# Optimization experiments

Hardware: AMD Instinct MI355X
Metric: run time of the kernel (lower is better)

## Reference

```python
import jax, jax.numpy as jnp
import numpy as np

B, S, D, H, HD = 2, 2048, 1024, 16, 64
K, L = 1024, 4  # num_codes, vq_levels


def setup_inputs() -> dict:
    key = jax.random.key(0)
    ks = jax.random.split(key, 12)
    w = lambda k, shape: jax.random.normal(k, shape, jnp.float32) * 0.02
    return {
        "x": jax.random.normal(ks[0], (B, S, D), jnp.float32),
        "ln1_g": jnp.ones((D,), jnp.float32), "ln1_b": jnp.zeros((D,), jnp.float32),
        "wq": w(ks[1], (D, D)), "wk": w(ks[2], (D, D)), "wv": w(ks[3], (D, D)),
        "wg": w(ks[4], (D, D)), "wo": w(ks[5], (D, D)),
        "ln2_g": jnp.ones((D,), jnp.float32), "ln2_b": jnp.zeros((D,), jnp.float32),
        "w1": w(ks[6], (D, 4 * D)), "b1": jnp.zeros((4 * D,), jnp.float32),
        "w2": w(ks[7], (4 * D, D)), "b2": jnp.zeros((D,), jnp.float32),
        "ln3_g": jnp.ones((D,), jnp.float32), "ln3_b": jnp.zeros((D,), jnp.float32),
        "codebooks": jax.random.uniform(ks[8], (L, K, D), jnp.float32, -1.0 / K, 1.0 / K),
    }


def _ln(x, g, b):
    m = jnp.mean(x, -1, keepdims=True)
    v = jnp.var(x, -1, keepdims=True)
    return (x - m) / jnp.sqrt(v + 1e-5) * g + b


def _rope(x):  # x: [B, S, H, HD]
    hd = x.shape[-1]
    inv = 1.0 / (10000.0 ** (jnp.arange(0, hd, 2, dtype=jnp.float32) / hd))
    t = jnp.arange(x.shape[1], dtype=jnp.float32)
    f = jnp.einsum('i,j->ij', t, inv)               # [S, HD/2]
    emb = jnp.concatenate([f, f], -1)               # [S, HD]
    cos = jnp.cos(emb)[None, :, None, :]
    sin = jnp.sin(emb)[None, :, None, :]
    x1, x2 = jnp.split(x, 2, -1)
    rot = jnp.concatenate([-x2, x1], -1)
    return x * cos + rot * sin


def reference(x, ln1_g, ln1_b, wq, wk, wv, wg, wo, ln2_g, ln2_b,
              w1, b1, w2, b2, ln3_g, ln3_b, codebooks):
    # --- retention sub-block (pre-LN) ---
    h = _ln(x, ln1_g, ln1_b)
    q = (h @ wq).reshape(B, S, H, HD)
    k = (h @ wk).reshape(B, S, H, HD)
    v = (h @ wv).reshape(B, S, H, HD)
    q, k = _rope(q), _rope(k)
    q, k, v = (a.transpose(0, 2, 1, 3) for a in (q, k, v))  # [B,H,S,HD]
    i = jnp.arange(S)
    dmask = jnp.tril(i[:, None] - i[None, :]).astype(jnp.float32)  # [S,S], >=0
    gamma = (1.0 - jnp.exp2(-5.0 - jnp.arange(H, dtype=jnp.float32)))[:, None, None]
    decay = (gamma ** dmask) * jnp.tril(jnp.ones((S, S), jnp.float32))  # [H,S,S]
    ret = jnp.einsum('bhqd,bhkd->bhqk', q, k) / np.sqrt(HD).astype(np.float32) * decay
    o = jnp.einsum('bhqk,bhkd->bhqd', ret, v).transpose(0, 2, 1, 3).reshape(B, S, D)
    g = jax.nn.silu(h @ wg)
    x = x + (o * g) @ wo
    # --- MLP sub-block (pre-LN) ---
    h2 = _ln(x, ln2_g, ln2_b)
    x = x + (jax.nn.gelu(h2 @ w1 + b1, approximate=False) @ w2 + b2)
    # --- residual vector quantizer ---
    xn = _ln(x, ln3_g, ln3_b)
    residual, total = xn, jnp.zeros_like(xn)
    ql, el = 0.0, 0.0
    for lvl in range(L):
        cb = codebooks[lvl]                         # [K, D]
        flat = residual.reshape(-1, D)              # [B*S, D]
        d2 = (jnp.sum(flat ** 2, 1, keepdims=True)
              + jnp.sum(cb ** 2, 1) - 2.0 * flat @ cb.T)
        idx = jnp.argmin(d2, 1)
        quant = cb[idx].reshape(xn.shape)
        ql = ql + jnp.mean((quant - jax.lax.stop_gradient(residual)) ** 2)
        el = el + jnp.mean((jax.lax.stop_gradient(quant) - residual) ** 2)
        total = total + quant
        residual = residual - jax.lax.stop_gradient(quant)
    final = xn + jax.lax.stop_gradient(total - xn)  # straight-through
    return (x + final, ql / L, el / L)
```

## Files before the change

kernel.cpp:

```cpp
#include <hip/hip_runtime.h>
#include <cstdint>
#include <cstddef>

#define DEV __device__ __forceinline__

typedef __attribute__((ext_vector_type(8))) short bf16x8;
typedef __attribute__((ext_vector_type(4))) float f32x4;

typedef const __attribute__((address_space(1))) void gl_void;
typedef __attribute__((address_space(3))) void lds_void;

DEV unsigned short f2bf(float f){
  union { float f; uint32_t u; } v; v.f = f;
  uint32_t r = v.u + 0x7FFFu + ((v.u >> 16) & 1u);
  return (unsigned short)(r >> 16);
}
DEV float bf2f(unsigned short u){
  union { uint32_t u; float f; } v; v.u = ((uint32_t)u) << 16; return v.f;
}
DEV uint32_t packbf2(float a, float b){
  return (uint32_t)f2bf(a) | ((uint32_t)f2bf(b) << 16);
}

__global__ void ln_kernel(const float* __restrict__ x, const float* __restrict__ gw,
                          const float* __restrict__ bw, unsigned short* __restrict__ obf,
                          float* __restrict__ of32)
{
  const int row = blockIdx.x, t = threadIdx.x;
  const float4 v = ((const float4*)(x + (size_t)row*1024))[t];
  float s  = v.x + v.y + v.z + v.w;
  float s2 = v.x*v.x + v.y*v.y + v.z*v.z + v.w*v.w;
  #pragma unroll
  for (int o = 32; o >= 1; o >>= 1){ s += __shfl_down(s, o); s2 += __shfl_down(s2, o); }
  __shared__ float red[8];
  const int w = t >> 6, ln = t & 63;
  if (ln == 0){ red[w] = s; red[4+w] = s2; }
  __syncthreads();
  const float fs  = red[0]+red[1]+red[2]+red[3];
  const float fs2 = red[4]+red[5]+red[6]+red[7];
  const float mean = fs * (1.0f/1024.0f);
  const float var  = fs2 * (1.0f/1024.0f) - mean*mean;
  const float rstd = rsqrtf(var + 1e-5f);
  const float4 gv = ((const float4*)gw)[t];
  const float4 bv = ((const float4*)bw)[t];
  float4 o4;
  o4.x = (v.x-mean)*rstd*gv.x + bv.x;
  o4.y = (v.y-mean)*rstd*gv.y + bv.y;
  o4.z = (v.z-mean)*rstd*gv.z + bv.z;
  o4.w = (v.w-mean)*rstd*gv.w + bv.w;
  if (of32) ((float4*)(of32 + (size_t)row*1024))[t] = o4;
  ushort4 ob; ob.x = f2bf(o4.x); ob.y = f2bf(o4.y); ob.z = f2bf(o4.z); ob.w = f2bf(o4.w);
  ((ushort4*)(obf + (size_t)row*1024))[t] = ob;
}

struct Ptr5 { const float* p[5]; };
__global__ void transpose_cvt5(Ptr5 in, unsigned short* __restrict__ out)
{
  __shared__ float tile[32][33];
  const float* src = in.p[blockIdx.z];
  unsigned short* dst = out + (size_t)blockIdx.z*1048576;
  const int c0 = blockIdx.x*32, r0 = blockIdx.y*32;
  const int tx = threadIdx.x & 31, ty = threadIdx.x >> 5;
  #pragma unroll
  for (int i = 0; i < 32; i += 8)
    tile[ty+i][tx] = src[(size_t)(r0+ty+i)*1024 + c0 + tx];
  __syncthreads();
  #pragma unroll
  for (int i = 0; i < 32; i += 8)
    dst[(size_t)(c0+ty+i)*1024 + r0 + tx] = f2bf(tile[tx][ty+i]);
}

__global__ void transpose_cvt(const float* __restrict__ in, unsigned short* __restrict__ out,
                              int R, int C)
{
  __shared__ float tile[32][33];
  const int c0 = blockIdx.x*32, r0 = blockIdx.y*32;
  const int tx = threadIdx.x & 31, ty = threadIdx.x >> 5;
  #pragma unroll
  for (int i = 0; i < 32; i += 8)
    tile[ty+i][tx] = in[(size_t)(r0+ty+i)*C + c0 + tx];
  __syncthreads();
  #pragma unroll
  for (int i = 0; i < 32; i += 8)
    out[(size_t)(c0+ty+i)*R + r0 + tx] = f2bf(tile[tx][ty+i]);
}

__global__ void cvtnorm_kernel(const float* __restrict__ cb, unsigned short* __restrict__ cbbf,
                               float* __restrict__ cbn2)
{
  const int code = blockIdx.x, t = threadIdx.x;
  const float4 v = ((const float4*)(cb + (size_t)code*1024))[t];
  ushort4 o; o.x = f2bf(v.x); o.y = f2bf(v.y); o.z = f2bf(v.z); o.w = f2bf(v.w);
  ((ushort4*)(cbbf + (size_t)code*1024))[t] = o;
  float s = v.x*v.x + v.y*v.y + v.z*v.z + v.w*v.w;
  #pragma unroll
  for (int off = 32; off >= 1; off >>= 1) s += __shfl_down(s, off);
  __shared__ float red[4];
  if ((t & 63) == 0) red[t >> 6] = s;
  __syncthreads();
  if (t == 0) cbn2[code] = red[0]+red[1]+red[2]+red[3];
}

__global__ void rope_tab(float2* __restrict__ rt)
{
  const int i = blockIdx.x*256 + threadIdx.x;
  const int s = i >> 5, j = i & 31;
  const float ang = (float)s * exp2f(-(float)j * 0.4152410118609203f);
  float sn, cs; sincosf(ang, &sn, &cs);
  rt[i] = make_float2(cs, sn);
}

template<int EPI>
__global__ __launch_bounds__(512, 2) void gemm256(
    const unsigned short* __restrict__ A, const unsigned short* __restrict__ BT,
    unsigned short* __restrict__ C, const float* __restrict__ bias,
    const float2* __restrict__ rt, int M, int N, int K)
{
  __shared__ __align__(16) unsigned short SH[65536];
  const int t = threadIdx.x;
  const int w = t >> 6, ln = t & 63, lg = ln >> 4, lc = ln & 15;
  const int wm = w >> 2, wn = w & 3;
  const int gx = gridDim.x, nwg = gridDim.x * gridDim.y;
  int lin = blockIdx.y * gx + blockIdx.x;
  lin = (lin >> 3) + (lin & 7) * (nwg >> 3);
  const int m0 = (lin / gx) * 256, n0 = (lin % gx) * 256;
  const int nkt = K >> 6;

  f32x4 acc[8][4] = {};

  auto stage = [&](int buf, int kt, int half, int isB){
    const unsigned short* src = isB ? BT : A;
    const int mb = isB ? n0 : m0;
    #pragma unroll
    for (int j = 0; j < 2; ++j){
      const int u = j*512 + t;
      const int ro = u >> 3;
      const int k16 = (u & 7) ^ (ro & 7);
      __builtin_amdgcn_global_load_lds(
        (gl_void*)(src + (size_t)(mb + half*128 + ro)*K + (size_t)kt*64 + k16*8),
        (lds_void*)&SH[buf*32768 + isB*16384 + half*8192 + (j*512 + (t & ~63))*8],
        16, 0, 0);
    }
  };

  auto ldA = [&](int buf, int mf, int ks) -> bf16x8 {
    const int R = wm*128 + mf*16 + lc;
    const int ci = (ks*32 + lg*8) ^ ((lc & 7) << 3);
    return *(const bf16x8*)&SH[buf*32768 + R*64 + ci];
  };
  auto ldB = [&](int buf, int nf, int ks) -> bf16x8 {
    const int R = wn*64 + nf*16 + lc;
    const int ci = (ks*32 + lg*8) ^ ((lc & 7) << 3);
    return *(const bf16x8*)&SH[buf*32768 + 16384 + R*64 + ci];
  };

  stage(0, 0, 0, 0); stage(0, 0, 1, 0); stage(0, 0, 0, 1); stage(0, 0, 1, 1);
  asm volatile("s_waitcnt vmcnt(0)" ::: "memory");
  __builtin_amdgcn_s_barrier();

  bf16x8 aF[4][2], bF[2][2];
  for (int kt = 0; kt < nkt; ++kt){
    const int cur = kt & 1;
    const bool pf = (kt + 1 < nkt);

    #pragma unroll
    for (int f = 0; f < 4; ++f){ aF[f][0] = ldA(cur, f, 0); aF[f][1] = ldA(cur, f, 1); }
    #pragma unroll
    for (int f = 0; f < 2; ++f){ bF[f][0] = ldB(cur, f, 0); bF[f][1] = ldB(cur, f, 1); }
    if (pf){ stage(cur^1, kt+1, 0, 0); stage(cur^1, kt+1, 0, 1); }
    __builtin_amdgcn_s_barrier();
    __builtin_amdgcn_s_setprio(1);
    #pragma unroll
    for (int mf = 0; mf < 4; ++mf)
      #pragma unroll
      for (int nf = 0; nf < 2; ++nf){
        acc[mf][nf] = __builtin_amdgcn_mfma_f32_16x16x32_bf16(aF[mf][0], bF[nf][0], acc[mf][nf], 0, 0, 0);
        acc[mf][nf] = __builtin_amdgcn_mfma_f32_16x16x32_bf16(aF[mf][1], bF[nf][1], acc[mf][nf], 0, 0, 0);
      }
    __builtin_amdgcn_s_setprio(0);
    __builtin_amdgcn_s_barrier();

    #pragma unroll
    for (int f = 0; f < 2; ++f){ bF[f][0] = ldB(cur, 2+f, 0); bF[f][1] = ldB(cur, 2+f, 1); }
    if (pf){ stage(cur^1, kt+1, 1, 1); stage(cur^1, kt+1, 1, 0); }
    __builtin_amdgcn_s_barrier();
    __builtin_amdgcn_s_setprio(1);
    #pragma unroll
    for (int mf = 0; mf < 4; ++mf)
      #pragma unroll
      for (int nf = 0; nf < 2; ++nf){
        acc[mf][2+nf] = __builtin_amdgcn_mfma_f32_16x16x32_bf16(aF[mf][0], bF[nf][0], acc[mf][2+nf], 0, 0, 0);
        acc[mf][2+nf] = __builtin_amdgcn_mfma_f32_16x16x32_bf16(aF[mf][1], bF[nf][1], acc[mf][2+nf], 0, 0, 0);
      }
    __builtin_amdgcn_s_setprio(0);
    __builtin_amdgcn_s_barrier();

    #pragma unroll
    for (int f = 0; f < 4; ++f){ aF[f][0] = ldA(cur, 4+f, 0); aF[f][1] = ldA(cur, 4+f, 1); }
    __builtin_amdgcn_s_barrier();
    __builtin_amdgcn_s_setprio(1);
    #pragma unroll
    for (int mf = 0; mf < 4; ++mf)
      #pragma unroll
      for (int nf = 0; nf < 2; ++nf){
        acc[4+mf][2+nf] = __builtin_amdgcn_mfma_f32_16x16x32_bf16(aF[mf][0], bF[nf][0], acc[4+mf][2+nf], 0, 0, 0);
        acc[4+mf][2+nf] = __builtin_amdgcn_mfma_f32_16x16x32_bf16(aF[mf][1], bF[nf][1], acc[4+mf][2+nf], 0, 0, 0);
      }
    __builtin_amdgcn_s_setprio(0);
    __builtin_amdgcn_s_barrier();

    #pragma unroll
    for (int f = 0; f < 2; ++f){ bF[f][0] = ldB(cur, f, 0); bF[f][1] = ldB(cur, f, 1); }
    __builtin_amdgcn_s_barrier();
    __builtin_amdgcn_s_setprio(1);
    #pragma unroll
    for (int mf = 0; mf < 4; ++mf)
      #pragma unroll
      for (int nf = 0; nf < 2; ++nf){
        acc[4+mf][nf] = __builtin_amdgcn_mfma_f32_16x16x32_bf16(aF[mf][0], bF[nf][0], acc[4+mf][nf], 0, 0, 0);
        acc[4+mf][nf] = __builtin_amdgcn_mfma_f32_16x16x32_bf16(aF[mf][1], bF[nf][1], acc[4+mf][nf], 0, 0, 0);
      }
    __builtin_amdgcn_s_setprio(0);
    asm volatile("s_waitcnt vmcnt(0)" ::: "memory");
    __builtin_amdgcn_s_barrier();
  }

  const int mrow = m0 + wm*128, ncol = n0 + wn*64;
  if constexpr (EPI == 3){
    const int sect = ncol >> 10;
    unsigned short* outp = C + (size_t)sect*4194304;
    #pragma unroll
    for (int mf = 0; mf < 8; ++mf){
      #pragma unroll
      for (int r = 0; r < 4; ++r){
        const int row = mrow + mf*16 + lg*4 + r;
        const int s_ = row & 2047;
        #pragma unroll
        for (int nf = 0; nf < 4; ++nf){
          const int c1 = (ncol + nf*16 + lc) & 1023;
          float v = acc[mf][nf][r];
          if (sect <= 1){
            const float2 cs = rt[(s_ << 5) + (c1 & 31)];
            const float vp = acc[mf][nf ^ 2][r];
            v = (c1 & 32) ? (v*cs.x + vp*cs.y) : (v*cs.x - vp*cs.y);
          } else if (sect == 3){
            v = v * (1.0f / (1.0f + __expf(-v)));
          }
          outp[(size_t)row*1024 + c1] = f2bf(v);
        }
      }
    }
  } else {
    #pragma unroll
    for (int mf = 0; mf < 8; ++mf){
      #pragma unroll
      for (int r = 0; r < 4; ++r){
        const int row = mrow + mf*16 + lg*4 + r;
        #pragma unroll
        for (int nf = 0; nf < 4; ++nf){
          const int col = ncol + nf*16 + lc;
          float v = acc[mf][nf][r] + bias[col];
          v = 0.5f * v * (1.0f + erff(v * 0.70710678118654752f));
          C[(size_t)row*N + col] = f2bf(v);
        }
      }
    }
  }
}

template<int EPI, bool BIAS, bool RES, bool OUTBF, int NSPLIT>
__global__ __launch_bounds__(256, 3) void gemm64_bt(
    const unsigned short* __restrict__ A, const unsigned short* __restrict__ BT,
    void* __restrict__ Cv, const float* __restrict__ bias, const float* __restrict__ resid,
    int M, int N, int K)
{
  __shared__ __align__(16) unsigned short As[2][64*64];
  __shared__ __align__(16) unsigned short Bs[2][128*64];
  const int t = threadIdx.x;
  const int w = t >> 6, ln = t & 63, lg = ln >> 4, lc = ln & 15;
  const int gx = gridDim.x, nwg = gridDim.x * gridDim.y;
  int lin = blockIdx.y * gx + blockIdx.x;
  lin = (lin >> 3) + (lin & 7) * (nwg >> 3);
  const int bx = lin % gx, by = lin / gx;
  const int m0 = by * 64, n0 = bx * 128;
  const int wr = (w >> 1) * 32, wc = (w & 1) * 64;
  f32x4 acc[2][4] = {};
  const int nkt = (K >> 6) / NSPLIT;
  const int ktb = (NSPLIT > 1) ? blockIdx.z * nkt : 0;

  auto stage = [&](int buf, int kt){
    #pragma unroll
    for (int c = 0; c < 2; ++c){
      const int chunk = c*256 + t;
      const int row = chunk >> 3;
      const int kb = (((chunk & 7) << 4) ^ ((row & 7) << 4)) >> 1;
      __builtin_amdgcn_global_load_lds(
          (gl_void*)(A + (size_t)(m0+row)*K + (size_t)(ktb+kt)*64 + kb),
          (lds_void*)&As[buf][(c*256 + w*64)*8], 16, 0, 0);
    }
    #pragma unroll
    for (int c = 0; c < 4; ++c){
      const int chunk = c*256 + t;
      const int row = chunk >> 3;
      const int kb = (((chunk & 7) << 4) ^ ((row & 7) << 4)) >> 1;
      __builtin_amdgcn_global_load_lds(
          (gl_void*)(BT + (size_t)(n0+row)*K + (size_t)(ktb+kt)*64 + kb),
          (lds_void*)&Bs[buf][(c*256 + w*64)*8], 16, 0, 0);
    }
  };

  stage(0, 0);
  __syncthreads();
  for (int kt = 0; kt < nkt; ++kt){
    const int cur = kt & 1;
    if (kt + 1 < nkt) stage(cur ^ 1, kt + 1);
    #pragma unroll
    for (int ks = 0; ks < 2; ++ks){
      bf16x8 af[2], bfr[4];
      #pragma unroll
      for (int i = 0; i < 2; ++i){
        const int rowA = wr + i*16 + lc;
        const int colA = (((ks<<6) + (lg<<4)) ^ ((rowA & 7) << 4)) >> 1;
        af[i] = *(const bf16x8*)&As[cur][rowA*64 + colA];
      }
      #pragma unroll
      for (int i = 0; i < 4; ++i){
        const int rowB = wc + i*16 + lc;
        const int colB = (((ks<<6) + (lg<<4)) ^ ((rowB & 7) << 4)) >> 1;
        bfr[i] = *(const bf16x8*)&Bs[cur][rowB*64 + colB];
      }
      #pragma unroll
      for (int m = 0; m < 2; ++m)
        #pragma unroll
        for (int n = 0; n < 4; ++n)
          acc[m][n] = __builtin_amdgcn_mfma_f32_16x16x32_bf16(af[m], bfr[n], acc[m][n], 0, 0, 0);
    }
    __syncthreads();
  }

  if constexpr (EPI == 4){
    #pragma unroll
    for (int m = 0; m < 2; ++m){
      #pragma unroll
      for (int r = 0; r < 4; ++r){
        float best = 3.4e38f; int bi = 0;
        #pragma unroll
        for (int n = 0; n < 4; ++n){
          const int col = n0 + wc + n*16 + lc;
          const float d = bias[col] - 2.0f*acc[m][n][r];
          if (d < best){ best = d; bi = col; }
        }
        #pragma unroll
        for (int o = 1; o < 16; o <<= 1){
          const float ob = __shfl_xor(best, o);
          const int oi = __shfl_xor(bi, o);
          if (ob < best || (ob == best && oi < bi)){ best = ob; bi = oi; }
        }
        if (lc == 0){
          const int row = m0 + wr + m*16 + lg*4 + r;
          ((float2*)Cv)[row*16 + bx*2 + (w & 1)] = make_float2(best, (float)bi);
        }
      }
    }
    return;
  }

  float* Cp = (float*)Cv + (NSPLIT > 1 ? (size_t)blockIdx.z * (size_t)M * N : 0);
  #pragma unroll
  for (int m = 0; m < 2; ++m){
    #pragma unroll
    for (int n = 0; n < 4; ++n){
      #pragma unroll
      for (int r = 0; r < 4; ++r){
        const int row = m0 + wr + m*16 + lg*4 + r;
        const int col = n0 + wc + n*16 + lc;
        float v = acc[m][n][r];
        if constexpr (BIAS) v += bias[col];
        if constexpr (RES) v += resid[(size_t)row*N + col];
        if constexpr (OUTBF) ((unsigned short*)Cv)[(size_t)row*N + col] = f2bf(v);
        else                 Cp[(size_t)row*N + col] = v;
      }
    }
  }
}

__global__ void splitk_reduce(const float* __restrict__ p, const float* __restrict__ bias,
                              const float* __restrict__ resid, float* __restrict__ out)
{
  const int i = blockIdx.x*256 + threadIdx.x;
  const float4 a = ((const float4*)p)[i];
  const float4 b = ((const float4*)(p + 4194304))[i];
  const float4 rv = ((const float4*)resid)[i];
  const float4 bv = ((const float4*)bias)[i & 255];
  float4 o;
  o.x = a.x + b.x + rv.x + bv.x;
  o.y = a.y + b.y + rv.y + bv.y;
  o.z = a.z + b.z + rv.z + bv.z;
  o.w = a.w + b.w + rv.w + bv.w;
  ((float4*)out)[i] = o;
}

__global__ __launch_bounds__(256, 2) void chunk_sum(
    const unsigned short* __restrict__ kb, const unsigned short* __restrict__ vb,
    float* __restrict__ Tbuf)
{
  __shared__ unsigned short KT[64*72];
  __shared__ unsigned short VT[64*72];
  const int t = threadIdx.x, w = t >> 6, ln = t & 63, lg = ln >> 4, lc = ln & 15;
  const int blk = blockIdx.x;
  const int bh = blk >> 5, c = blk & 31;
  const int b = bh >> 4, hh = bh & 15;
  const float lg2g = log2f(1.0f - exp2f(-5.0f - (float)hh));
  #pragma unroll
  for (int ch = 0; ch < 2; ++ch){
    const int chunk = ch*256 + t;
    const int i = chunk >> 3, d0 = (chunk & 7)*8;
    const size_t gofs = ((size_t)(b*2048 + c*64 + i))*1024 + hh*64 + d0;
    const float wi = exp2f(lg2g * (float)(64 - i));
    union {uint4 u; unsigned short s[8];} kv, vv;
    kv.u = *(const uint4*)(kb + gofs);
    vv.u = *(const uint4*)(vb + gofs);
    #pragma unroll
    for (int j = 0; j < 8; ++j){
      KT[(d0+j)*72 + i] = f2bf(bf2f(kv.s[j]) * wi);
      VT[(d0+j)*72 + i] = vv.s[j];
    }
  }
  __syncthreads();
  f32x4 acc[4] = {};
  #pragma unroll
  for (int ks = 0; ks < 2; ++ks){
    const bf16x8 af = *(const bf16x8*)&KT[(w*16 + lc)*72 + ks*32 + lg*8];
    #pragma unroll
    for (int n = 0; n < 4; ++n){
      const bf16x8 bf = *(const bf16x8*)&VT[(n*16 + lc)*72 + ks*32 + lg*8];
      acc[n] = __builtin_amdgcn_mfma_f32_16x16x32_bf16(af, bf, acc[n], 0, 0, 0);
    }
  }
  float* out = Tbuf + (size_t)blk*4096;
  #pragma unroll
  for (int n = 0; n < 4; ++n)
    #pragma unroll
    for (int r = 0; r < 4; ++r)
      out[(w*16 + lg*4 + r)*64 + n*16 + lc] = acc[n][r];
}

__global__ void chunk_scan(const float* __restrict__ Tbuf, unsigned short* __restrict__ statesT)
{
  const int bh = blockIdx.x, t = threadIdx.x;
  const int hh = bh & 15;
  const float gamma = 1.0f - exp2f(-5.0f - (float)hh);
  const float g64 = exp2f(log2f(gamma) * 64.0f);
  float S[16];
  #pragma unroll
  for (int j = 0; j < 16; ++j) S[j] = 0.f;
  const int dv = t >> 2, d0 = (t & 3) * 16;
  for (int c = 0; c < 32; ++c){
    const size_t base = ((size_t)(bh*32 + c))*4096;
    union { unsigned short s[8]; uint4 u; } p0, p1;
    #pragma unroll
    for (int j = 0; j < 8; ++j){ p0.s[j] = f2bf(S[j]); p1.s[j] = f2bf(S[8+j]); }
    *(uint4*)(statesT + base + t*16)     = p0.u;
    *(uint4*)(statesT + base + t*16 + 8) = p1.u;
    #pragma unroll
    for (int j = 0; j < 16; ++j)
      S[j] = g64*S[j] + Tbuf[base + (size_t)(d0 + j)*64 + dv];
  }
}

__global__ __launch_bounds__(256, 2) void retention_chunk(
    const unsigned short* __restrict__ qb, const unsigned short* __restrict__ kb,
    const unsigned short* __restrict__ vb, const unsigned short* __restrict__ gb,
    const unsigned short* __restrict__ statesT, unsigned short* __restrict__ og)
{
  __shared__ unsigned short VT[64*72];
  __shared__ unsigned short Pw[64*72];
  const int t = threadIdx.x, w = t >> 6, ln = t & 63, lg = ln >> 4, lc = ln & 15;
  const int blk = blockIdx.x;
  const int bh = blk >> 5, c = blk & 31;
  const int b = bh >> 4, hh = bh & 15;
  const float lg2g = log2f(1.0f - exp2f(-5.0f - (float)hh));
  float gpr[4];
  #pragma unroll
  for (int r = 0; r < 4; ++r) gpr[r] = exp2f(-lg2g * (float)r);
  const size_t rowbase = (size_t)(b*2048 + c*64);

  #pragma unroll
  for (int ch = 0; ch < 2; ++ch){
    const int chunk = ch*256 + t;
    const int i = chunk >> 3, d0 = (chunk & 7)*8;
    union {uint4 u; unsigned short s[8];} vv;
    vv.u = *(const uint4*)(vb + (rowbase + i)*1024 + hh*64 + d0);
    #pragma unroll
    for (int j = 0; j < 8; ++j) VT[(d0+j)*72 + i] = vv.s[j];
  }

  bf16x8 Qf[2], Kf[4][2];
  #pragma unroll
  for (int ks = 0; ks < 2; ++ks){
    union {uint4 u; bf16x8 f;} cv;
    cv.u = *(const uint4*)(qb + (rowbase + w*16 + lc)*1024 + hh*64 + ks*32 + lg*8);
    Qf[ks] = cv.f;
    #pragma unroll
    for (int mt = 0; mt < 4; ++mt){
      union {uint4 u; bf16x8 f;} kv;
      kv.u = *(const uint4*)(kb + (rowbase + mt*16 + lc)*1024 + hh*64 + ks*32 + lg*8);
      Kf[mt][ks] = kv.f;
    }
  }

  f32x4 st[4] = {};
  #pragma unroll
  for (int ks = 0; ks < 2; ++ks)
    #pragma unroll
    for (int mt = 0; mt < 4; ++mt)
      st[mt] = __builtin_amdgcn_mfma_f32_16x16x32_bf16(Kf[mt][ks], Qf[ks], st[mt], 0, 0, 0);

  __syncthreads();

  #pragma unroll
  for (int mt = 0; mt < 4; ++mt){
    const int kp = mt*16 + lg*4;
    const int qrow = w*16 + lc;
    const int delta0 = qrow - kp;
    const float dec0 = exp2f(lg2g * (float)delta0) * 0.125f;
    float vals[4];
    #pragma unroll
    for (int r = 0; r < 4; ++r)
      vals[r] = (delta0 >= r) ? st[mt][r] * dec0 * gpr[r] : 0.0f;
    uint2 pk; pk.x = packbf2(vals[0], vals[1]); pk.y = packbf2(vals[2], vals[3]);
    *(uint2*)&Pw[qrow*72 + kp] = pk;
  }

  f32x4 acc[4] = {};
  const unsigned short* Sbase = statesT + (size_t)blk*4096;
  #pragma unroll
  for (int ks = 0; ks < 2; ++ks)
    #pragma unroll
    for (int n = 0; n < 4; ++n){
      union {uint4 u; bf16x8 f;} sv;
      sv.u = *(const uint4*)(Sbase + (n*16 + lc)*64 + ks*32 + lg*8);
      acc[n] = __builtin_amdgcn_mfma_f32_16x16x32_bf16(Qf[ks], sv.f, acc[n], 0, 0, 0);
    }
  #pragma unroll
  for (int n = 0; n < 4; ++n)
    #pragma unroll
    for (int r = 0; r < 4; ++r)
      acc[n][r] *= exp2f(lg2g * (float)(w*16 + lg*4 + r)) * 0.125f;

  #pragma unroll
  for (int ks = 0; ks < 2; ++ks){
    const bf16x8 Pf = *(const bf16x8*)&Pw[(w*16 + lc)*72 + ks*32 + lg*8];
    #pragma unroll
    for (int n = 0; n < 4; ++n){
      const bf16x8 Vf = *(const bf16x8*)&VT[(n*16 + lc)*72 + ks*32 + lg*8];
      acc[n] = __builtin_amdgcn_mfma_f32_16x16x32_bf16(Pf, Vf, acc[n], 0, 0, 0);
    }
  }

  #pragma unroll
  for (int n = 0; n < 4; ++n){
    #pragma unroll
    for (int r = 0; r < 4; ++r){
      const size_t row = rowbase + w*16 + lg*4 + r;
      const int col = hh*64 + n*16 + lc;
      const float gv = bf2f(gb[row*1024 + col]);
      og[row*1024 + col] = f2bf(acc[n][r] * gv);
    }
  }
}

__global__ void rvq_update3(const float* __restrict__ cb_l, const float2* __restrict__ partials,
                            const float* __restrict__ res_in, float* __restrict__ res_out,
                            unsigned short* __restrict__ resb, float* __restrict__ qlpart, int lvl)
{
  const int m = blockIdx.x, t = threadIdx.x;
  __shared__ int sid;
  if (t == 0){
    float best = 3.4e38f; int bi = 0;
    #pragma unroll
    for (int p = 0; p < 16; ++p){
      const float2 pr = partials[m*16 + p];
      if (pr.x < best){ best = pr.x; bi = (int)pr.y; }
    }
    sid = bi;
  }
  __syncthreads();
  const int id = sid;
  const float4 qv = ((const float4*)(cb_l + (size_t)id*1024))[t];
  const float4 rv = ((const float4*)(res_in + (size_t)m*1024))[t];
  float4 nr; nr.x = rv.x - qv.x; nr.y = rv.y - qv.y; nr.z = rv.z - qv.z; nr.w = rv.w - qv.w;
  ((float4*)(res_out + (size_t)m*1024))[t] = nr;
  ushort4 nb; nb.x = f2bf(nr.x); nb.y = f2bf(nr.y); nb.z = f2bf(nr.z); nb.w = f2bf(nr.w);
  ((ushort4*)(resb + (size_t)m*1024))[t] = nb;
  float s = nr.x*nr.x + nr.y*nr.y + nr.z*nr.z + nr.w*nr.w;
  #pragma unroll
  for (int o = 32; o >= 1; o >>= 1) s += __shfl_down(s, o);
  __shared__ float red[4];
  if ((t & 63) == 0) red[t >> 6] = s;
  __syncthreads();
  if (t == 0) qlpart[lvl*4096 + m] = red[0]+red[1]+red[2]+red[3];
}

__global__ void final_add3(const float* __restrict__ x2, const float* __restrict__ xn,
                           const float* __restrict__ res4, float* __restrict__ out)
{
  const int i = blockIdx.x*256 + threadIdx.x;
  const float4 a = ((const float4*)x2)[i];
  const float4 b = ((const float4*)xn)[i];
  const float4 c = ((const float4*)res4)[i];
  float4 o;
  o.x = a.x + b.x - c.x;
  o.y = a.y + b.y - c.y;
  o.z = a.z + b.z - c.z;
  o.w = a.w + b.w - c.w;
  ((float4*)out)[i] = o;
}

__global__ void ql_final(const float* __restrict__ qlpart, float* __restrict__ outs)
{
  const int t = threadIdx.x;
  float s = 0.f;
  for (int i = t; i < 16384; i += 256) s += qlpart[i];
  #pragma unroll
  for (int o = 32; o >= 1; o >>= 1) s += __shfl_down(s, o);
  __shared__ float red[4];
  if ((t & 63) == 0) red[t >> 6] = s;
  __syncthreads();
  if (t == 0){
    const float q = (red[0]+red[1]+red[2]+red[3]) * (1.0f/4194304.0f) * 0.25f;
    outs[0] = q; outs[1] = q;
  }
}

extern "C" void kernel_launch(void* const* d_in, const int* in_sizes, int n_in,
                              void* d_out, int out_size, void* d_ws, size_t ws_size,
                              hipStream_t stream)
{
  const float* x     = (const float*)d_in[0];
  const float* ln1_g = (const float*)d_in[1];
  const float* ln1_b = (const float*)d_in[2];
  const float* wq    = (const float*)d_in[3];
  const float* wk    = (const float*)d_in[4];
  const float* wv    = (const float*)d_in[5];
  const float* wg    = (const float*)d_in[6];
  const float* wo    = (const float*)d_in[7];
  const float* ln2_g = (const float*)d_in[8];
  const float* ln2_b = (const float*)d_in[9];
  const float* w1    = (const float*)d_in[10];
  const float* b1    = (const float*)d_in[11];
  const float* w2    = (const float*)d_in[12];
  const float* b2    = (const float*)d_in[13];
  const float* ln3_g = (const float*)d_in[14];
  const float* ln3_b = (const float*)d_in[15];
  const float* cb    = (const float*)d_in[16];

  char* ws = (char*)d_ws;
  const size_t MB = 1024*1024;
  unsigned short* wqkvgT = (unsigned short*)(ws + 0*MB);
  unsigned short* w1T  = (unsigned short*)(ws + 10*MB);
  unsigned short* w2T  = (unsigned short*)(ws + 18*MB);
  unsigned short* cbbf = (unsigned short*)(ws + 26*MB);
  float* cbn2     = (float*)(ws + 34*MB);
  float* qlpart   = (float*)(ws + 34*MB + 16*1024);
  float2* partials= (float2*)(ws + 34*MB + 128*1024);
  unsigned short* hbf  = (unsigned short*)(ws + 35*MB);
  unsigned short* qbuf = (unsigned short*)(ws + 43*MB);
  unsigned short* kbuf = (unsigned short*)(ws + 51*MB);
  unsigned short* vbuf = (unsigned short*)(ws + 59*MB);
  unsigned short* gbuf = (unsigned short*)(ws + 67*MB);
  float* skbuf  = (float*)(ws + 43*MB);
  unsigned short* ogb  = (unsigned short*)(ws + 75*MB);
  float* x1     = (float*)(ws + 83*MB);
  unsigned short* h2   = (unsigned short*)(ws + 99*MB);
  unsigned short* a1   = (unsigned short*)(ws + 107*MB);
  float* x2     = (float*)(ws + 139*MB);
  float* Tbuf   = (float*)(ws + 139*MB);
  float* xnf    = (float*)(ws + 155*MB);
  unsigned short* statesT = (unsigned short*)(ws + 155*MB);
  unsigned short* resb = (unsigned short*)(ws + 171*MB);
  float2* rtab  = (float2*)(ws + 179*MB);
  float* resw   = (float*)(ws + 187*MB);

  float* outf = (float*)d_out;

  Ptr5 p5; p5.p[0]=wq; p5.p[1]=wk; p5.p[2]=wv; p5.p[3]=wg; p5.p[4]=wo;
  hipLaunchKernelGGL(transpose_cvt5, dim3(32,32,5), dim3(256), 0, stream, p5, wqkvgT);
  hipLaunchKernelGGL(transpose_cvt, dim3(128,32), dim3(256), 0, stream, w1, w1T, 1024, 4096);
  hipLaunchKernelGGL(transpose_cvt, dim3(32,128), dim3(256), 0, stream, w2, w2T, 4096, 1024);
  hipLaunchKernelGGL(cvtnorm_kernel, dim3(4096), dim3(256), 0, stream, cb, cbbf, cbn2);
  hipLaunchKernelGGL(rope_tab, dim3(256), dim3(256), 0, stream, rtab);

  hipLaunchKernelGGL(ln_kernel, dim3(4096), dim3(256), 0, stream, x, ln1_g, ln1_b, hbf, (float*)nullptr);
  hipLaunchKernelGGL((gemm256<3>), dim3(16,16), dim3(512), 0, stream,
                     hbf, wqkvgT, qbuf, (const float*)nullptr, (const float2*)rtab, 4096, 4096, 1024);
  hipLaunchKernelGGL(chunk_sum,  dim3(1024), dim3(256), 0, stream, kbuf, vbuf, Tbuf);
  hipLaunchKernelGGL(chunk_scan, dim3(32),   dim3(256), 0, stream, Tbuf, statesT);
  hipLaunchKernelGGL(retention_chunk, dim3(1024), dim3(256), 0, stream,
                     qbuf, kbuf, vbuf, gbuf, statesT, ogb);
  hipLaunchKernelGGL((gemm64_bt<0,false,true,false,1>), dim3(8,64), dim3(256), 0, stream,
                     ogb, wqkvgT + 4194304, (void*)x1, (const float*)nullptr, x, 4096, 1024, 1024);

  hipLaunchKernelGGL(ln_kernel, dim3(4096), dim3(256), 0, stream, x1, ln2_g, ln2_b, h2, (float*)nullptr);
  hipLaunchKernelGGL((gemm256<2>), dim3(16,16), dim3(512), 0, stream,
                     h2, w1T, a1, b1, (const float2*)rtab, 4096, 4096, 1024);
  hipLaunchKernelGGL((gemm64_bt<0,false,false,false,2>), dim3(8,64,2), dim3(256), 0, stream,
                     a1, w2T, (void*)skbuf, (const float*)nullptr, (const float*)nullptr, 4096, 1024, 4096);
  hipLaunchKernelGGL(splitk_reduce, dim3(4096), dim3(256), 0, stream, skbuf, b2, x1, x2);

  hipLaunchKernelGGL(ln_kernel, dim3(4096), dim3(256), 0, stream, x2, ln3_g, ln3_b, resb, xnf);
  for (int lvl = 0; lvl < 4; ++lvl){
    hipLaunchKernelGGL((gemm64_bt<4,false,false,false,1>), dim3(8,64), dim3(256), 0, stream,
                       resb, cbbf + (size_t)lvl*1048576, (void*)partials,
                       cbn2 + lvl*1024, (const float*)nullptr, 4096, 1024, 1024);
    hipLaunchKernelGGL(rvq_update3, dim3(4096), dim3(256), 0, stream,
                       cb + (size_t)lvl*1048576, partials,
                       (lvl == 0) ? xnf : resw, resw, resb, qlpart, lvl);
  }

  hipLaunchKernelGGL(final_add3, dim3(4096), dim3(256), 0, stream, x2, xnf, resw, outf);
  hipLaunchKernelGGL(ql_final, dim3(1), dim3(256), 0, stream, qlpart, outf + 4194304);
}
```

Baseline: 435.9 us.

## Triple-buffer GEMM LDS stages with two-ahead prefetch and partial vmcnt waits

New measurement: 446.4 us. 1.02x slower.

```diff
diff --git a/kernel.cpp b/kernel.cpp
--- a/kernel.cpp
+++ b/kernel.cpp
@@ -116,7 +116,7 @@
     unsigned short* __restrict__ C, const float* __restrict__ bias,
     const float2* __restrict__ rt, int M, int N, int K)
 {
-  __shared__ __align__(16) unsigned short SH[65536];
+  __shared__ __align__(16) unsigned short SH[49152];
   const int t = threadIdx.x;
   const int w = t >> 6, ln = t & 63, lg = ln >> 4, lc = ln & 15;
   const int wm = w >> 2, wn = w & 3;
@@ -124,104 +124,75 @@
   int lin = blockIdx.y * gx + blockIdx.x;
   lin = (lin >> 3) + (lin & 7) * (nwg >> 3);
   const int m0 = (lin / gx) * 256, n0 = (lin % gx) * 256;
-  const int nkt = K >> 6;
+  const int nkt = K >> 5;
 
   f32x4 acc[8][4] = {};
 
-  auto stage = [&](int buf, int kt, int half, int isB){
-    const unsigned short* src = isB ? BT : A;
-    const int mb = isB ? n0 : m0;
-    #pragma unroll
-    for (int j = 0; j < 2; ++j){
-      const int u = j*512 + t;
-      const int ro = u >> 3;
-      const int k16 = (u & 7) ^ (ro & 7);
-      __builtin_amdgcn_global_load_lds(
-        (gl_void*)(src + (size_t)(mb + half*128 + ro)*K + (size_t)kt*64 + k16*8),
-        (lds_void*)&SH[buf*32768 + isB*16384 + half*8192 + (j*512 + (t & ~63))*8],
-        16, 0, 0);
+  auto stage = [&](int buf, int kt){
+    #pragma unroll
+    for (int isB = 0; isB < 2; ++isB){
+      const unsigned short* src = isB ? BT : A;
+      const int mb = isB ? n0 : m0;
+      #pragma unroll
+      for (int j = 0; j < 2; ++j){
+        const int u = j*512 + t;
+        const int ro = u >> 2;
+        const int su = (u & 3) ^ ((ro >> 1) & 3);
+        __builtin_amdgcn_global_load_lds(
+          (gl_void*)(src + (size_t)(mb + ro)*K + (size_t)kt*32 + su*8),
+          (lds_void*)&SH[buf*16384 + isB*8192 + (j*512 + (t & ~63))*8],
+          16, 0, 0);
+      }
     }
   };
 
-  auto ldA = [&](int buf, int mf, int ks) -> bf16x8 {
+  auto ldA = [&](int buf, int mf) -> bf16x8 {
     const int R = wm*128 + mf*16 + lc;
-    const int ci = (ks*32 + lg*8) ^ ((lc & 7) << 3);
-    return *(const bf16x8*)&SH[buf*32768 + R*64 + ci];
+    const int cu = lg ^ ((R >> 1) & 3);
+    return *(const bf16x8*)&SH[buf*16384 + (R*4 + cu)*8];
   };
-  auto ldB = [&](int buf, int nf, int ks) -> bf16x8 {
+  auto ldB = [&](int buf, int nf) -> bf16x8 {
     const int R = wn*64 + nf*16 + lc;
-    const int ci = (ks*32 + lg*8) ^ ((lc & 7) << 3);
-    return *(const bf16x8*)&SH[buf*32768 + 16384 + R*64 + ci];
+    const int cu = lg ^ ((R >> 1) & 3);
+    return *(const bf16x8*)&SH[buf*16384 + 8192 + (R*4 + cu)*8];
   };
 
-  stage(0, 0, 0, 0); stage(0, 0, 1, 0); stage(0, 0, 0, 1); stage(0, 0, 1, 1);
-  asm volatile("s_waitcnt vmcnt(0)" ::: "memory");
+  stage(0, 0); stage(1, 1);
+  asm volatile("s_waitcnt vmcnt(4)" ::: "memory");
   __builtin_amdgcn_s_barrier();
 
-  bf16x8 aF[4][2], bF[2][2];
   for (int kt = 0; kt < nkt; ++kt){
-    const int cur = kt & 1;
-    const bool pf = (kt + 1 < nkt);
-
-    #pragma unroll
-    for (int f = 0; f < 4; ++f){ aF[f][0] = ldA(cur, f, 0); aF[f][1] = ldA(cur, f, 1); }
-    #pragma unroll
-    for (int f = 0; f < 2; ++f){ bF[f][0] = ldB(cur, f, 0); bF[f][1] = ldB(cur, f, 1); }
-    if (pf){ stage(cur^1, kt+1, 0, 0); stage(cur^1, kt+1, 0, 1); }
+    const int cur = kt % 3;
+    const bool pf = (kt + 2 < nkt);
+    bf16x8 aF[4], bF[4];
+
+    if (pf) stage((kt + 2) % 3, kt + 2);
+    #pragma unroll
+    for (int f = 0; f < 4; ++f){ aF[f] = ldA(cur, f); bF[f] = ldB(cur, f); }
     __builtin_amdgcn_s_barrier();
     __builtin_amdgcn_s_setprio(1);
     #pragma unroll
     for (int mf = 0; mf < 4; ++mf)
       #pragma unroll
-      for (int nf = 0; nf < 2; ++nf){
-        acc[mf][nf] = __builtin_amdgcn_mfma_f32_16x16x32_bf16(aF[mf][0], bF[nf][0], acc[mf][nf], 0, 0, 0);
-        acc[mf][nf] = __builtin_amdgcn_mfma_f32_16x16x32_bf16(aF[mf][1], bF[nf][1], acc[mf][nf], 0, 0, 0);
-      }
+      for (int nf = 0; nf < 4; ++nf)
+        acc[mf][nf] = __builtin_amdgcn_mfma_f32_16x16x32_bf16(aF[mf], bF[nf], acc[mf][nf], 0, 0, 0);
     __builtin_amdgcn_s_setprio(0);
+    asm volatile("s_waitcnt lgkmcnt(0)" ::: "memory");
     __builtin_amdgcn_s_barrier();
 
     #pragma unroll
-    for (int f = 0; f < 2; ++f){ bF[f][0] = ldB(cur, 2+f, 0); bF[f][1] = ldB(cur, 2+f, 1); }
-    if (pf){ stage(cur^1, kt+1, 1, 1); stage(cur^1, kt+1, 1, 0); }
+    for (int f = 0; f < 4; ++f) aF[f] = ldA(cur, 4 + f);
     __builtin_amdgcn_s_barrier();
     __builtin_amdgcn_s_setprio(1);
     #pragma unroll
     for (int mf = 0; mf < 4; ++mf)
       #pragma unroll
-      for (int nf = 0; nf < 2; ++nf){
-        acc[mf][2+nf] = __builtin_amdgcn_mfma_f32_16x16x32_bf16(aF[mf][0], bF[nf][0], acc[mf][2+nf], 0, 0, 0);
-        acc[mf][2+nf] = __builtin_amdgcn_mfma_f32_16x16x32_bf16(aF[mf][1], bF[nf][1], acc[mf][2+nf], 0, 0, 0);
-      }
+      for (int nf = 0; nf < 4; ++nf)
+        acc[4+mf][nf] = __builtin_amdgcn_mfma_f32_16x16x32_bf16(aF[mf], bF[nf], acc[4+mf][nf], 0, 0, 0);
     __builtin_amdgcn_s_setprio(0);
-    __builtin_amdgcn_s_barrier();
-
-    #pragma unroll
-    for (int f = 0; f < 4; ++f){ aF[f][0] = ldA(cur, 4+f, 0); aF[f][1] = ldA(cur, 4+f, 1); }
-    __builtin_amdgcn_s_barrier();
-    __builtin_amdgcn_s_setprio(1);
-    #pragma unroll
-    for (int mf = 0; mf < 4; ++mf)
-      #pragma unroll
-      for (int nf = 0; nf < 2; ++nf){
-        acc[4+mf][2+nf] = __builtin_amdgcn_mfma_f32_16x16x32_bf16(aF[mf][0], bF[nf][0], acc[4+mf][2+nf], 0, 0, 0);
-        acc[4+mf][2+nf] = __builtin_amdgcn_mfma_f32_16x16x32_bf16(aF[mf][1], bF[nf][1], acc[4+mf][2+nf], 0, 0, 0);
-      }
-    __builtin_amdgcn_s_setprio(0);
-    __builtin_amdgcn_s_barrier();
-
-    #pragma unroll
-    for (int f = 0; f < 2; ++f){ bF[f][0] = ldB(cur, f, 0); bF[f][1] = ldB(cur, f, 1); }
-    __builtin_amdgcn_s_barrier();
-    __builtin_amdgcn_s_setprio(1);
-    #pragma unroll
-    for (int mf = 0; mf < 4; ++mf)
-      #pragma unroll
-      for (int nf = 0; nf < 2; ++nf){
-        acc[4+mf][nf] = __builtin_amdgcn_mfma_f32_16x16x32_bf16(aF[mf][0], bF[nf][0], acc[4+mf][nf], 0, 0, 0);
-        acc[4+mf][nf] = __builtin_amdgcn_mfma_f32_16x16x32_bf16(aF[mf][1], bF[nf][1], acc[4+mf][nf], 0, 0, 0);
-      }
-    __builtin_amdgcn_s_setprio(0);
-    asm volatile("s_waitcnt vmcnt(0)" ::: "memory");
+    asm volatile("s_waitcnt lgkmcnt(0)" ::: "memory");
+    if (pf) asm volatile("s_waitcnt vmcnt(4)" ::: "memory");
+    else    asm volatile("s_waitcnt vmcnt(0)" ::: "memory");
     __builtin_amdgcn_s_barrier();
   }
 
@@ -269,13 +240,13 @@
 }
 
 template<int EPI, bool BIAS, bool RES, bool OUTBF, int NSPLIT>
-__global__ __launch_bounds__(256, 3) void gemm64_bt(
+__global__ __launch_bounds__(256, 2) void gemm64_bt(
     const unsigned short* __restrict__ A, const unsigned short* __restrict__ BT,
     void* __restrict__ Cv, const float* __restrict__ bias, const float* __restrict__ resid,
     int M, int N, int K)
 {
-  __shared__ __align__(16) unsigned short As[2][64*64];
-  __shared__ __align__(16) unsigned short Bs[2][128*64];
+  __shared__ __align__(16) unsigned short As[3][64*64];
+  __shared__ __align__(16) unsigned short Bs[3][128*64];
   const int t = threadIdx.x;
   const int w = t >> 6, ln = t & 63, lg = ln >> 4, lc = ln & 15;
   const int gx = gridDim.x, nwg = gridDim.x * gridDim.y;
@@ -309,11 +280,15 @@
     }
   };
 
-  stage(0, 0);
-  __syncthreads();
+  stage(0, 0); stage(1, 1);
+  asm volatile("s_waitcnt vmcnt(6)" ::: "memory");
+  __builtin_amdgcn_s_barrier();
+
   for (int kt = 0; kt < nkt; ++kt){
-    const int cur = kt & 1;
-    if (kt + 1 < nkt) stage(cur ^ 1, kt + 1);
+    const int cur = kt % 3;
+    const bool pf = (kt + 2 < nkt);
+    if (pf) stage((kt + 2) % 3, kt + 2);
+    __builtin_amdgcn_s_setprio(1);
     #pragma unroll
     for (int ks = 0; ks < 2; ++ks){
       bf16x8 af[2], bfr[4];
@@ -335,7 +310,11 @@
         for (int n = 0; n < 4; ++n)
           acc[m][n] = __builtin_amdgcn_mfma_f32_16x16x32_bf16(af[m], bfr[n], acc[m][n], 0, 0, 0);
     }
-    __syncthreads();
+    __builtin_amdgcn_s_setprio(0);
+    asm volatile("s_waitcnt lgkmcnt(0)" ::: "memory");
+    if (pf) asm volatile("s_waitcnt vmcnt(6)" ::: "memory");
+    else    asm volatile("s_waitcnt vmcnt(0)" ::: "memory");
+    __builtin_amdgcn_s_barrier();
   }
 
   if constexpr (EPI == 4){
```
